# Performance work log

Measured on AMD Instinct MI355X. Metric: run time of the kernel, lower is better.

The kernel has to match this reference:

```python
import jax, jax.numpy as jnp
import numpy as np
import math

B, T, D, S, V = 128, 32, 64, 32, 8192
MAX_REC = 8
PONDER = 0.01
TWO_PI = 2.0 * math.pi


def setup_inputs():
    key = jax.random.key(0)
    ks = jax.random.split(key, 12)
    sd = 1.0 / math.sqrt(D)
    g = lambda k, shape, s: jax.random.normal(k, shape, jnp.float32) * s
    return {
        "x_seq": jax.random.randint(ks[0], (B, T), 0, V),
        "encoder_emb": g(ks[1], (V, 2 * D), 0.02),
        "vq_emb": g(ks[2], (V, 2 * D), sd),
        "norm_rg": jnp.ones((D,), jnp.float32), "norm_rb": jnp.zeros((D,), jnp.float32),
        "norm_ig": jnp.ones((D,), jnp.float32), "norm_ib": jnp.zeros((D,), jnp.float32),
        "qkv_Wr": g(ks[3], (3, D, D), sd), "qkv_br": g(ks[4], (3, D), sd),
        "qkv_Wi": g(ks[5], (3, D, D), sd), "qkv_bi": g(ks[6], (3, D), sd),
        "gate_w": g(ks[7], (2 * D,), sd), "gate_b": jnp.zeros((), jnp.float32),
        "arb_W": g(ks[8], (3, 2 * D), sd), "arb_b": jnp.zeros((3,), jnp.float32),
        "dec_W": g(ks[9], (V, 2 * D), sd), "dec_b": jnp.zeros((V,), jnp.float32),
        "halt_bias": jnp.asarray(3.0, jnp.float32),
        "input_gate": jnp.asarray(0.0, jnp.float32),
    }


def _ln(x, g, b, eps=1e-5):
    mu = x.mean(-1, keepdims=True)
    var = ((x - mu) ** 2).mean(-1, keepdims=True)
    return (x - mu) * jax.lax.rsqrt(var + eps) * g + b


def _forward(x_seq, encoder_emb, vq_emb, norm_rg, norm_rb, norm_ig, norm_ib,
             qkv_Wr, qkv_br, qkv_Wi, qkv_bi, gate_w, gate_b, arb_W, arb_b,
             dec_W, dec_b, halt_bias, input_gate):
    sg = jax.lax.stop_gradient
    e_sq = (vq_emb ** 2).sum(-1)  # [V]
    alpha = jax.nn.sigmoid(input_gate)
    bias = jax.nn.softplus(halt_bias)

    def clin(xr, xi, Wr, br, Wi, bi):
        # torch ComplexLinear: real = fc_r(xr) - fc_i(xi); imag = fc_r(xi) + fc_i(xr)
        return (xr @ Wr.T + br) - (xi @ Wi.T + bi), (xi @ Wr.T + br) + (xr @ Wi.T + bi)

    def mem_write(gr, gi, mr, mi):
        flat = jnp.concatenate([gr, gi], -1)
        wg = jax.nn.sigmoid(flat @ gate_w + gate_b)[:, None, None]  # [B,1,1]
        shr, shi = jnp.roll(mr, 1, axis=1), jnp.roll(mi, 1, axis=1)
        hr = wg * gr[:, None, :] + (1.0 - wg) * shr[:, :1]
        hi = wg * gi[:, None, :] + (1.0 - wg) * shi[:, :1]
        return jnp.concatenate([hr, shr[:, 1:]], 1), jnp.concatenate([hi, shi[:, 1:]], 1)

    def time_step(carry, xt):
        gw_r, gw_i, mem_r, mem_i = carry
        x_r, x_i = xt
        gw_r = alpha * gw_r + (1.0 - alpha) * x_r
        gw_i = alpha * gw_i + (1.0 - alpha) * x_i
        active = jnp.ones((B,), jnp.float32)
        acc_vq = jnp.zeros((B,), jnp.float32)
        acc_ent = jnp.zeros((B,), jnp.float32)
        acc_pond = jnp.zeros((B,), jnp.float32)
        acc_ph = jnp.zeros((B,), jnp.float32)
        fin_idx = jnp.zeros((B,), jnp.int32)
        prev_ang = jnp.arctan2(gw_i, gw_r)
        for _ in range(MAX_REC):
            cr = _ln(gw_r, norm_rg, norm_rb)
            ci = _ln(gw_i, norm_ig, norm_ib)
            z_flat = jnp.concatenate([cr, ci], -1)  # [B,2D]
            # squared-euclidean scores; argmin identical to cdist argmin
            d2 = (z_flat ** 2).sum(-1, keepdims=True) - 2.0 * (z_flat @ vq_emb.T) + e_sq
            idx = jnp.argmin(d2, -1).astype(jnp.int32)
            z_q = vq_emb[idx]
            vq_loss = ((z_q - sg(z_flat)) ** 2).mean(-1) + 0.25 * ((sg(z_q) - z_flat) ** 2).mean(-1)
            z_st = z_flat + sg(z_q - z_flat)  # straight-through
            counts = jnp.zeros((V,), jnp.float32).at[idx].add(1.0) / B
            entropy = -(counts * jnp.log(counts + 1e-10)).sum()
            v_r, v_i = z_st[:, :D], z_st[:, D:]
            # Hermitian gating
            qr, qi = clin(cr, ci, qkv_Wr[0], qkv_br[0], qkv_Wi[0], qkv_bi[0])
            kr, ki = clin(cr, ci, qkv_Wr[1], qkv_br[1], qkv_Wi[1], qkv_bi[1])
            vr2, vi2 = clin(cr, ci, qkv_Wr[2], qkv_br[2], qkv_Wi[2], qkv_bi[2])
            gate = jax.nn.sigmoid((qr * kr + qi * ki).sum(-1, keepdims=True))
            g_r, g_i = vr2 * gate, vi2 * gate
            # memory read (Re<m, q> attention over slots)
            sim = jnp.einsum('bsd,bd->bs', mem_r, cr) + jnp.einsum('bsd,bd->bs', mem_i, ci)
            attn = jax.nn.softmax(sim, -1)
            m_r = jnp.einsum('bs,bsd->bd', attn, mem_r)
            m_i = jnp.einsum('bs,bsd->bd', attn, mem_i)
            gates = jax.nn.softmax(z_flat @ arb_W.T + arb_b, -1)  # [B,3]
            upd_r = gates[:, 0:1] * g_r + gates[:, 1:2] * m_r + gates[:, 2:3] * v_r
            upd_i = gates[:, 0:1] * g_i + gates[:, 1:2] * m_i + gates[:, 2:3] * v_i
            cand_r = 0.6 * cr + 0.4 * upd_r
            cand_i = 0.6 * ci + 0.4 * upd_i
            ang = jnp.arctan2(cand_i, cand_r)
            diff = jnp.abs(ang - prev_ang)
            diff = jnp.minimum(diff, TWO_PI - diff)
            acc_ph = acc_ph + active * diff.mean(-1)
            prev_ang = ang
            halt_prob = jax.nn.sigmoid(bias - vq_loss)
            should_stop = (halt_prob > 0.5).astype(jnp.float32)
            acc_pond = acc_pond + active * PONDER
            mflat = active > 0.5
            acc_vq = jnp.where(mflat, vq_loss, acc_vq)
            acc_ent = jnp.where(mflat, entropy, acc_ent)
            fin_idx = jnp.where(mflat, idx, fin_idx)
            am = mflat[:, None]
            gw_r = jnp.where(am, cand_r, gw_r)
            gw_i = jnp.where(am, cand_i, gw_i)
            active = active * (1.0 - should_stop)
        mem_r, mem_i = mem_write(gw_r, gw_i, mem_r, mem_i)
        stats_t = jnp.stack([acc_vq.mean(), acc_ent.mean(), acc_pond.mean(), acc_ph.mean()])
        return (gw_r, gw_i, mem_r, mem_i), (gw_r, gw_i, fin_idx, stats_t)

    emb = encoder_emb[x_seq]  # [B,T,2D]
    xr = jnp.transpose(emb[..., :D], (1, 0, 2))  # [T,B,D]
    xi = jnp.transpose(emb[..., D:], (1, 0, 2))
    init = (jnp.zeros((B, D), jnp.float32), jnp.zeros((B, D), jnp.float32),
            jnp.zeros((B, S, D), jnp.float32), jnp.zeros((B, S, D), jnp.float32))
    _, (out_r, out_i, idxs, stats) = jax.lax.scan(time_step, init, (xr, xi))
    out = jnp.concatenate([jnp.transpose(out_r, (1, 0, 2)),
                           jnp.transpose(out_i, (1, 0, 2))], -1)  # [B,T,2D]
    logits = out @ dec_W.T + dec_b  # [B,T,V]
    return logits, stats.sum(0) / T, jnp.transpose(idxs)  # [B,T]


def reference(x_seq, encoder_emb, vq_emb, norm_rg, norm_rb, norm_ig, norm_ib, qkv_Wr, qkv_br, qkv_Wi, qkv_bi, gate_w, gate_b, arb_W, arb_b, dec_W, dec_b, halt_bias, input_gate):
    return _forward(x_seq, encoder_emb, vq_emb, norm_rg, norm_rb, norm_ig, norm_ib,
                    qkv_Wr, qkv_br, qkv_Wi, qkv_bi, gate_w, gate_b, arb_W, arb_b,
                    dec_W, dec_b, halt_bias, input_gate)
```

## Files before the change

kernel.cpp:

```cpp
#include <hip/hip_runtime.h>
#include <math.h>

#define TT 32
#define MAXREC 8
#define NBLK 256
#define NTHR 512

#define OFF_ZBUF   0u
#define OFF_ZBUFB  65536u
#define OFF_KEYS   98304u
#define OFF_ZDONE  229376u
#define OFF_ESQ    231424u
#define OFF_RST    264192u
#define OFF_OUTHB  266240u
#define OFF_WB     1314816u

#define SENT 0x7FFFFFFFu
#define IDXM 0x1FFFu
#define LOGN 33554432u
#define TWO_PI_F 6.283185307179586f

typedef float f32x4 __attribute__((ext_vector_type(4)));
typedef short bf16x8 __attribute__((ext_vector_type(8)));
typedef unsigned long long u64;

__device__ __forceinline__ float wredsum(float v) {
#pragma unroll
  for (int m = 32; m > 0; m >>= 1) v += __shfl_xor(v, m);
  return v;
}
__device__ __forceinline__ u64 shflx64(u64 v, int m) {
  int lo = __shfl_xor((int)(unsigned)(v & 0xffffffffull), m);
  int hi = __shfl_xor((int)(unsigned)(v >> 32), m);
  return ((u64)(unsigned)hi << 32) | (unsigned)lo;
}
__device__ __forceinline__ u64 packkey(float d, unsigned c) {
  unsigned u = __float_as_uint(d);
  u = (u & 0x80000000u) ? ~u : (u | 0x80000000u);
  return ((u64)u << 32) | c;
}
__device__ __forceinline__ float unpackd2(u64 key) {
  unsigned hi = (unsigned)(key >> 32);
  unsigned orig = (hi & 0x80000000u) ? (hi & 0x7fffffffu) : ~hi;
  return __uint_as_float(orig);
}
__device__ __forceinline__ unsigned short f2bf(float f) {
  unsigned u = __float_as_uint(f);
  unsigned r = (u >> 16) & 1u;
  u += 0x7fffu + r;
  return (unsigned short)(u >> 16);
}

__device__ __forceinline__ u64 ld_coh64(const u64* p) {
  u64 v;
  asm volatile("global_load_dwordx2 %0, %1, off sc0 sc1\n\ts_waitcnt vmcnt(0)"
               : "=&v"(v) : "v"(p) : "memory");
  return v;
}
__device__ __forceinline__ void st_coh_f32(float* p, float v) {
  asm volatile("global_store_dword %0, %1, off sc0 sc1" :: "v"(p), "v"(v) : "memory");
}
__device__ __forceinline__ void st_coh32(unsigned* p, unsigned v) {
  asm volatile("global_store_dword %0, %1, off sc0 sc1" :: "v"(p), "v"(v) : "memory");
}
__device__ __forceinline__ void st_coh64(u64* p, u64 v) {
  asm volatile("global_store_dwordx2 %0, %1, off sc0 sc1" :: "v"(p), "v"(v) : "memory");
}
__device__ __forceinline__ void drain_vm() {
  asm volatile("s_waitcnt vmcnt(0)" ::: "memory");
}
__device__ __forceinline__ void ld4w(const float* base,
    unsigned o0, unsigned o1, unsigned o2, unsigned o3,
    f32x4& a0, f32x4& a1, f32x4& a2, f32x4& a3) {
  asm volatile(
      "global_load_dwordx4 %0, %4, %8 sc0 sc1\n\t"
      "global_load_dwordx4 %1, %5, %8 sc0 sc1\n\t"
      "global_load_dwordx4 %2, %6, %8 sc0 sc1\n\t"
      "global_load_dwordx4 %3, %7, %8 sc0 sc1\n\t"
      "s_waitcnt vmcnt(0)"
      : "=&v"(a0), "=&v"(a1), "=&v"(a2), "=&v"(a3)
      : "v"(o0), "v"(o1), "v"(o2), "v"(o3), "s"(base)
      : "memory");
}
__device__ __forceinline__ void ld8w(const float* base,
    unsigned o0, unsigned o1, unsigned o2, unsigned o3,
    unsigned o4, unsigned o5, unsigned o6, unsigned o7,
    f32x4& a0, f32x4& a1, f32x4& a2, f32x4& a3,
    f32x4& a4, f32x4& a5, f32x4& a6, f32x4& a7) {
  asm volatile(
      "global_load_dwordx4 %0, %8, %16 sc0 sc1\n\t"
      "global_load_dwordx4 %1, %9, %16 sc0 sc1\n\t"
      "global_load_dwordx4 %2, %10, %16 sc0 sc1\n\t"
      "global_load_dwordx4 %3, %11, %16 sc0 sc1\n\t"
      "global_load_dwordx4 %4, %12, %16 sc0 sc1\n\t"
      "global_load_dwordx4 %5, %13, %16 sc0 sc1\n\t"
      "global_load_dwordx4 %6, %14, %16 sc0 sc1\n\t"
      "global_load_dwordx4 %7, %15, %16 sc0 sc1\n\t"
      "s_waitcnt vmcnt(0)"
      : "=&v"(a0), "=&v"(a1), "=&v"(a2), "=&v"(a3),
        "=&v"(a4), "=&v"(a5), "=&v"(a6), "=&v"(a7)
      : "v"(o0), "v"(o1), "v"(o2), "v"(o3),
        "v"(o4), "v"(o5), "v"(o6), "v"(o7),
        "s"(base)
      : "memory");
}

__global__ __launch_bounds__(512) void sacrsn_init(char* __restrict__ ws) {
  u64* zd = (u64*)(ws + OFF_ZDONE);
  if (threadIdx.x < 256) zd[threadIdx.x] = 0ull;
}

__global__ __launch_bounds__(256) void k_prepv(const float* __restrict__ vqe,
                                               char* __restrict__ ws) {
  unsigned short* vqeB = (unsigned short*)(ws + OFF_WB);
  float* esqG = (float*)(ws + OFF_ESQ);
  const int i = (blockIdx.x * 256 + threadIdx.x) * 4;
  float4 v = *(const float4*)(vqe + i);
  ushort4 o;
  o.x = f2bf(v.x); o.y = f2bf(v.y); o.z = f2bf(v.z); o.w = f2bf(v.w);
  *(ushort4*)(vqeB + i) = o;
  if (blockIdx.x < 32) {
    const int c = blockIdx.x * 256 + threadIdx.x;
    const float4* e = (const float4*)(vqe + ((size_t)c << 7));
    float s = 0.f;
#pragma unroll 8
    for (int k4 = 0; k4 < 32; ++k4) {
      float4 q = e[k4];
      s = fmaf(q.x, q.x, fmaf(q.y, q.y, fmaf(q.z, q.z, fmaf(q.w, q.w, s))));
    }
    esqG[c] = s;
  }
}

__global__ __launch_bounds__(256) void k_prepd(const float* __restrict__ dW,
                                               char* __restrict__ ws) {
  unsigned short* dWb = (unsigned short*)(ws + OFF_WB);
  const int i = (blockIdx.x * 256 + threadIdx.x) * 4;
  float4 v = *(const float4*)(dW + i);
  ushort4 o;
  o.x = f2bf(v.x); o.y = f2bf(v.y); o.z = f2bf(v.z); o.w = f2bf(v.w);
  *(ushort4*)(dWb + i) = o;
}

__global__ __launch_bounds__(NTHR) void sacrsn_main(
    const int* __restrict__ x_seq, const float* __restrict__ enc,
    const float* __restrict__ vqe,
    const float* __restrict__ nrg, const float* __restrict__ nrb,
    const float* __restrict__ nig, const float* __restrict__ nib,
    const float* __restrict__ qWr, const float* __restrict__ qbr,
    const float* __restrict__ qWi, const float* __restrict__ qbi,
    const float* __restrict__ gtw, const float* __restrict__ gtb,
    const float* __restrict__ aW, const float* __restrict__ ab,
    const float* __restrict__ hbp, const float* __restrict__ igp,
    float* __restrict__ dout, char* __restrict__ ws)
{
  float* zbuf = (float*)(ws + OFF_ZBUF);
  unsigned* zbufB32 = (unsigned*)(ws + OFF_ZBUFB);
  u64*   keys = (u64*)(ws + OFF_KEYS);
  u64*   zdone64 = (u64*)(ws + OFF_ZDONE);
  u64*   finalA = (u64*)(ws + OFF_ZDONE + 8u);
  const float* esqG = (const float*)(ws + OFF_ESQ);
  const unsigned short* vqeB = (const unsigned short*)(ws + OFF_WB);
  unsigned short* outhB = (unsigned short*)(ws + OFF_OUTHB);
  float* rst  = (float*)(ws + OFF_RST);

  const int tid = threadIdx.x;
  const int wv = tid >> 6, ln = tid & 63;
  const int blk = blockIdx.x;
  const bool owner = (blk < 128);

  __shared__ float memLr[32 * 65];
  __shared__ float memLi[32 * 65];
  __shared__ float gwrowL[128], pangL[64], zfmL[128], zqL[128];
  __shared__ float qkL[6][64], simL[32], attnL[32], mrL[64], miL[64];
  __shared__ unsigned idxL[128] __attribute__((aligned(16)));
  __shared__ u64 key128L[128], kred[128];
  __shared__ float arbWL[3 * 128];
  __shared__ float scalL[8], entpL[2], vqpL[2], wsumL[2], z2pL[2];
  __shared__ float accL[4], totL[4];
  __shared__ float dmeanS;
  __shared__ u64 actM[2], actN[2];
  __shared__ float z2L[128], sz2L[128];
  __shared__ u64 rowminU[128];
  __shared__ unsigned candL[8192];
  __shared__ unsigned candCount;

  const float alpha = 1.0f / (1.0f + expf(-igp[0]));
  const float onema = 1.0f - alpha;
  const float hbias = log1pf(expf(hbp[0]));
  const float gtb0 = gtb[0];

  if (!owner) {
    const int s = blk - 128;
    const int w = tid >> 6, l = tid & 63;
    const int ar = l & 15, kg = l >> 4;
    const int rowbase = w * 16;
    if (tid < 128) rowminU[tid] = ~0ull;
    if (tid == 0) candCount = 0u;
    __syncthreads();
    unsigned k = 0;
    while (true) {
      u64 tv;
      bool done;
      {
        const u64* tp = &zdone64[(size_t)(rowbase + ar) * 2];
        bool sent;
        while (true) {
          tv = ld_coh64(tp);
          unsigned lo = (unsigned)tv;
          sent = (lo == SENT);
          bool ok = (lo == k + 1u) || sent;
          if (__all(ok)) break;
          __builtin_amdgcn_s_sleep(1);
        }
        done = __any(sent);
      }
      if (done) break;
      {
        float z2 = __uint_as_float((unsigned)(tv >> 32));
        z2L[rowbase + ar] = z2;
        sz2L[rowbase + ar] = sqrtf(z2);
      }
      f32x4 af0, af1, af2, af3;
      {
        const unsigned rb = (unsigned)((rowbase + ar) * 256 + kg * 16);
        ld4w((const float*)(ws + OFF_ZBUFB), rb, rb + 64u, rb + 128u, rb + 192u,
             af0, af1, af2, af3);
      }
      bf16x8 afr[4];
      afr[0] = *(bf16x8*)&af0; afr[1] = *(bf16x8*)&af1;
      afr[2] = *(bf16x8*)&af2; afr[3] = *(bf16x8*)&af3;
      f32x4 dc[4];
#pragma unroll
      for (int nt = 0; nt < 4; ++nt) dc[nt] = (f32x4){0.f, 0.f, 0.f, 0.f};
#pragma unroll
      for (int kc = 0; kc < 4; ++kc) {
#pragma unroll
        for (int nt = 0; nt < 4; ++nt) {
          bf16x8 b = *(const bf16x8*)(vqeB + (((size_t)(s * 64 + nt * 16 + ar)) << 7)
                                      + kc * 32 + kg * 8);
          dc[nt] = __builtin_amdgcn_mfma_f32_16x16x32_bf16(afr[kc], b, dc[nt], 0, 0, 0);
        }
      }
      float aV[4][4], eV[4][4], Lmin[4];
#pragma unroll
      for (int rr = 0; rr < 4; ++rr) Lmin[rr] = 1e30f;
#pragma unroll
      for (int nt = 0; nt < 4; ++nt) {
        const int code = s * 64 + nt * 16 + ar;
        const float es = esqG[code];
        const float se = sqrtf(es);
#pragma unroll
        for (int rr = 0; rr < 4; ++rr) {
          const int row = rowbase + kg * 4 + rr;
          float av = (z2L[row] - 2.0f * dc[nt][rr]) + es;
          float ev = fmaf(0.0082f * sz2L[row], se, 1e-3f);
          aV[nt][rr] = av; eV[nt][rr] = ev;
          float ae = av + ev;
          if (ae < Lmin[rr]) Lmin[rr] = ae;
        }
      }
#pragma unroll
      for (int m2 = 1; m2 < 16; m2 <<= 1)
#pragma unroll
        for (int rr = 0; rr < 4; ++rr) {
          float o = __shfl_xor(Lmin[rr], m2);
          if (o < Lmin[rr]) Lmin[rr] = o;
        }
#pragma unroll
      for (int nt = 0; nt < 4; ++nt)
#pragma unroll
        for (int rr = 0; rr < 4; ++rr)
          if (aV[nt][rr] - eV[nt][rr] <= Lmin[rr]) {
            const unsigned row = (unsigned)(rowbase + kg * 4 + rr);
            const unsigned code = (unsigned)(s * 64 + nt * 16 + ar);
            unsigned pos = atomicAdd(&candCount, 1u);
            candL[pos] = (row << 16) | code;
          }
      __syncthreads();
      const unsigned cnt = candCount;
      for (unsigned base = 0; base < cnt; base += 128u) {
        const unsigned eI = base + (unsigned)(tid >> 2);
        const int sub = tid & 3;
        const bool valid = eI < cnt;
        float dsum = 0.f;
        int row = 0, code = 0;
        if (valid) {
          unsigned en = candL[eI];
          row = (int)(en >> 16); code = (int)(en & 0xFFFFu);
          f32x4 zv0, zv1, zv2, zv3, zv4, zv5, zv6, zv7;
          const unsigned zb = (unsigned)(row * 512 + sub * 128);
          ld8w(zbuf, zb, zb + 16u, zb + 32u, zb + 48u,
               zb + 64u, zb + 80u, zb + 96u, zb + 112u,
               zv0, zv1, zv2, zv3, zv4, zv5, zv6, zv7);
          const float4* ep = (const float4*)(vqe + ((size_t)code << 7) + sub * 32);
          float4 e0 = ep[0], e1 = ep[1], e2 = ep[2], e3 = ep[3];
          float4 e4 = ep[4], e5 = ep[5], e6 = ep[6], e7 = ep[7];
          dsum = fmaf(zv0[0], e0.x, fmaf(zv0[1], e0.y, fmaf(zv0[2], e0.z, fmaf(zv0[3], e0.w, 0.f))));
          dsum = fmaf(zv1[0], e1.x, fmaf(zv1[1], e1.y, fmaf(zv1[2], e1.z, fmaf(zv1[3], e1.w, dsum))));
          dsum = fmaf(zv2[0], e2.x, fmaf(zv2[1], e2.y, fmaf(zv2[2], e2.z, fmaf(zv2[3], e2.w, dsum))));
          dsum = fmaf(zv3[0], e3.x, fmaf(zv3[1], e3.y, fmaf(zv3[2], e3.z, fmaf(zv3[3], e3.w, dsum))));
          dsum = fmaf(zv4[0], e4.x, fmaf(zv4[1], e4.y, fmaf(zv4[2], e4.z, fmaf(zv4[3], e4.w, dsum))));
          dsum = fmaf(zv5[0], e5.x, fmaf(zv5[1], e5.y, fmaf(zv5[2], e5.z, fmaf(zv5[3], e5.w, dsum))));
          dsum = fmaf(zv6[0], e6.x, fmaf(zv6[1], e6.y, fmaf(zv6[2], e6.z, fmaf(zv6[3], e6.w, dsum))));
          dsum = fmaf(zv7[0], e7.x, fmaf(zv7[1], e7.y, fmaf(zv7[2], e7.z, fmaf(zv7[3], e7.w, dsum))));
        }
        dsum += __shfl_xor(dsum, 1);
        dsum += __shfl_xor(dsum, 2);
        if (valid && sub == 0) {
          float d2 = (z2L[row] - 2.0f * dsum) + esqG[code];
          atomicMin(&rowminU[row], packkey(d2, (unsigned)code));
        }
      }
      __syncthreads();
      if (tid < 128) {
        u64 kk = rowminU[tid];
        rowminU[tid] = ~0ull;
        if (tid == 0) candCount = 0u;
        st_coh64(&keys[(size_t)s * 128 + tid], kk | ((u64)(k + 1u) << 13));
      }
      k++;
    }
    return;
  }

  float lnG = 0.0f, lnB = 0.0f, gtwv = 0.0f;
  if (tid < 64) { lnG = nrg[tid]; lnB = nrb[tid]; }
  else if (tid < 128) { lnG = nig[tid - 64]; lnB = nib[tid - 64]; }
  if (tid < 128) gtwv = gtw[tid];
  for (int i = tid; i < 32 * 65; i += NTHR) { memLr[i] = 0.0f; memLi[i] = 0.0f; }
  if (tid < 4) { totL[tid] = 0.0f; accL[tid] = 0.0f; }
  if (tid < 2) actM[tid] = ~0ull;
  for (int i = tid; i < 384; i += NTHR) arbWL[i] = aW[i];
  {
    int tok = x_seq[blk * TT];
    if (tid < 128) gwrowL[tid] = onema * enc[((size_t)tok << 7) + tid];
  }
  __syncthreads();
  if (tid < 64) pangL[tid] = atan2f(gwrowL[64 + tid], gwrowL[tid]);
  if (tid < 128) {
    float val = gwrowL[tid];
    float mu = wredsum(val) * 0.015625f;
    float xc = val - mu;
    float vr = wredsum(xc * xc) * 0.015625f;
    float z = xc * (1.0f / sqrtf(vr + 1e-5f)) * lnG + lnB;
    zfmL[tid] = z;
    st_coh_f32(&zbuf[(blk << 7) + tid], z);
    float zo = __shfl_xor(z, 1);
    if ((tid & 1) == 0) {
      unsigned pk = (unsigned)f2bf(z) | ((unsigned)f2bf(zo) << 16);
      st_coh32(&zbufB32[blk * 64 + (tid >> 1)], pk);
    }
    float s2 = wredsum(z * z);
    if (ln == 0) z2pL[wv] = s2;
  }
  drain_vm();
  __syncthreads();
  if (tid == 0) {
    float z2 = z2pL[0] + z2pL[1];
    st_coh64(&zdone64[blk * 2], (u64)1u | ((u64)__float_as_uint(z2) << 32));
  }

  int t = 0, it = 0;
  unsigned k = 0;
  for (;;) {
    const unsigned tag = k + 1u;
    float encN = 0.0f;
    {
      int tnext = (t + 1 < TT) ? t + 1 : t;
      if (tid < 128) {
        int tk = x_seq[blk * TT + tnext];
        encN = enc[((size_t)tk << 7) + tid];
      }
    }
    if (tid < 192) {
      const int h = tid >> 6, j = tid & 63;
      const float* wr = qWr + h * 4096 + j * 64;
      const float* wi = qWi + h * 4096 + j * 64;
      float da = 0.0f, db_ = 0.0f, dc2 = 0.0f, de = 0.0f;
#pragma unroll 4
      for (int d4 = 0; d4 < 64; d4 += 4) {
        float4 wrv = *(const float4*)&wr[d4];
        float4 wiv = *(const float4*)&wi[d4];
        float4 crv = *(const float4*)&zfmL[d4];
        float4 civ = *(const float4*)&zfmL[64 + d4];
        da = fmaf(crv.x, wrv.x, fmaf(crv.y, wrv.y, fmaf(crv.z, wrv.z, fmaf(crv.w, wrv.w, da))));
        db_ = fmaf(civ.x, wiv.x, fmaf(civ.y, wiv.y, fmaf(civ.z, wiv.z, fmaf(civ.w, wiv.w, db_))));
        dc2 = fmaf(civ.x, wrv.x, fmaf(civ.y, wrv.y, fmaf(civ.z, wrv.z, fmaf(civ.w, wrv.w, dc2))));
        de = fmaf(crv.x, wiv.x, fmaf(crv.y, wiv.y, fmaf(crv.z, wiv.z, fmaf(crv.w, wiv.w, de))));
      }
      float brv = qbr[h * 64 + j], biv = qbi[h * 64 + j];
      qkL[2 * h][j] = da + brv - db_ - biv;
      qkL[2 * h + 1][j] = dc2 + brv + de + biv;
    } else if (tid < 224) {
      const int s2 = tid - 192;
      float a2 = 0.0f;
      for (int d = 0; d < 64; ++d)
        a2 = fmaf(memLr[s2 * 65 + d], zfmL[d], fmaf(memLi[s2 * 65 + d], zfmL[64 + d], a2));
      simL[s2] = a2;
    } else if (tid < 227) {
      const int h = tid - 224;
      float a2 = ab[h];
      for (int k2 = 0; k2 < 128; ++k2) a2 = fmaf(zfmL[k2], arbWL[h * 128 + k2], a2);
      scalL[3 + h] = a2;
    }
    __syncthreads();
    if (tid < 64) {
      float p = fmaf(qkL[0][tid], qkL[2][tid], qkL[1][tid] * qkL[3][tid]);
      p = wredsum(p);
      if (tid == 0) scalL[0] = 1.0f / (1.0f + expf(-p));
    } else if (tid < 96) {
      const int s2 = tid - 64;
      float v = simL[s2];
      float m = v;
#pragma unroll
      for (int msk = 16; msk > 0; msk >>= 1) m = fmaxf(m, __shfl_xor(m, msk));
      float e = expf(v - m);
      float ss = e;
#pragma unroll
      for (int msk = 16; msk > 0; msk >>= 1) ss += __shfl_xor(ss, msk);
      attnL[s2] = e / ss;
    } else if (tid == 96) {
      float a0 = scalL[3], a1 = scalL[4], a2 = scalL[5];
      float m = fmaxf(a0, fmaxf(a1, a2));
      float e0 = expf(a0 - m), e1 = expf(a1 - m), e2 = expf(a2 - m);
      float ssum = e0 + e1 + e2;
      scalL[3] = e0 / ssum; scalL[4] = e1 / ssum; scalL[5] = e2 / ssum;
    }
    __syncthreads();
    if (tid < 128) {
      const int d = ln;
      const float* ml = (wv == 0) ? memLr : memLi;
      float a2 = 0.0f;
#pragma unroll 4
      for (int s2 = 0; s2 < 32; ++s2) a2 = fmaf(attnL[s2], ml[s2 * 65 + d], a2);
      if (wv == 0) mrL[d] = a2; else miL[d] = a2;
    }
    if (tid < 128) {
      const u64* kp = &keys[(size_t)tid * 128 + blk];
      u64 v;
      while (true) {
        v = ld_coh64(kp);
        if (__all(((unsigned)(v >> 13) & 0x7FFFFu) == tag)) break;
        __builtin_amdgcn_s_sleep(1);
      }
      kred[tid] = v;
    }
    __syncthreads();
    if (tid < 64) {
      u64 a = kred[tid], b = kred[tid + 64];
      if (b < a) a = b;
#pragma unroll
      for (int m2 = 32; m2 > 0; m2 >>= 1) { u64 o = shflx64(a, m2); if (o < a) a = o; }
      if (tid == 0) st_coh64(&finalA[blk * 2], a);
    }
    if (tid < 128) {
      const u64* fp = &finalA[(size_t)tid * 2];
      u64 v;
      while (true) {
        v = ld_coh64(fp);
        if (__all(((unsigned)(v >> 13) & 0x7FFFFu) == tag)) break;
        __builtin_amdgcn_s_sleep(1);
      }
      key128L[tid] = v;
    }
    __syncthreads();
    const bool aoldb = ((actM[blk >> 6] >> (blk & 63)) & 1ull) != 0ull;
    if (tid < 128) {
      u64 key = key128L[tid];
      idxL[tid] = (unsigned)key & IDXM;
      float d2 = unpackd2(key);
      bool act_b = ((actM[tid >> 6] >> (tid & 63)) & 1ull) != 0ull;
      bool stop = (1.25f * 0.0078125f * d2) < hbias;
      u64 ball = __ballot(act_b && !stop);
      if (ln == 0) actN[tid >> 6] = ball;
    } else if (tid < 256) {
      const int d = tid - 128;
      unsigned ii2 = (unsigned)key128L[blk] & IDXM;
      float zq = vqe[((size_t)ii2 << 7) + d];
      zqL[d] = zq;
      float df = zq - zfmL[d];
      float sm = wredsum(df * df);
      if (ln == 0) vqpL[wv - 2] = sm;
    }
    __syncthreads();
    const bool anyAct = (actN[0] | actN[1]) != 0ull;
    const bool mf = aoldb;
    if (tid < 2) actM[tid] = actN[tid];
    if (tid < 64) {
      const int d = tid;
      float gate = scalL[0], g0 = scalL[3], g1 = scalL[4], g2 = scalL[5];
      float cr = zfmL[d], ci = zfmL[64 + d];
      float ur = fmaf(g0, qkL[4][d] * gate, fmaf(g1, mrL[d], g2 * zqL[d]));
      float ui = fmaf(g0, qkL[5][d] * gate, fmaf(g1, miL[d], g2 * zqL[64 + d]));
      float cdr = fmaf(0.4f, ur, 0.6f * cr);
      float cdi = fmaf(0.4f, ui, 0.6f * ci);
      mrL[d] = cdr; miL[d] = cdi;
      if (mf) { gwrowL[d] = cdr; gwrowL[64 + d] = cdi; }
    }
    __syncthreads();
    const bool newT = !(anyAct && it < MAXREC - 1);
    const bool finished = newT && (t == TT - 1);
    if (newT && !finished) {
      float pr = 0.0f;
      if (tid < 128) {
        pr = gwrowL[tid];
        outhB[((size_t)blk * TT + t) * 128 + tid] = f2bf(pr);
        float part = wredsum(pr * gtwv);
        if (ln == 0) wsumL[wv] = part;
      }
      __syncthreads();
      if (tid < 128) {
        float wg = 1.0f / (1.0f + expf(-(wsumL[0] + wsumL[1] + gtb0)));
        int slot = 31 - t;
        float* m = (tid < 64) ? &memLr[slot * 65 + tid] : &memLi[slot * 65 + (tid - 64)];
        *m = fmaf(wg, pr, (1.0f - wg) * (*m));
        gwrowL[tid] = fmaf(alpha, pr, onema * encN);
      }
      __syncthreads();
    }
    if (!finished) {
      if (tid < 128) {
        float val = gwrowL[tid];
        float mu = wredsum(val) * 0.015625f;
        float xc = val - mu;
        float vr = wredsum(xc * xc) * 0.015625f;
        float z = xc * (1.0f / sqrtf(vr + 1e-5f)) * lnG + lnB;
        zfmL[tid] = z;
        st_coh_f32(&zbuf[(blk << 7) + tid], z);
        float zo = __shfl_xor(z, 1);
        if ((tid & 1) == 0) {
          unsigned pk = (unsigned)f2bf(z) | ((unsigned)f2bf(zo) << 16);
          st_coh32(&zbufB32[blk * 64 + (tid >> 1)], pk);
        }
        float s2 = wredsum(z * z);
        if (ln == 0) z2pL[wv] = s2;
      }
      drain_vm();
      __syncthreads();
      if (tid == 0) {
        float z2 = z2pL[0] + z2pL[1];
        st_coh64(&zdone64[blk * 2], (u64)(k + 2u) | ((u64)__float_as_uint(z2) << 32));
      }
    } else {
      __syncthreads();
    }
    if (tid < 64) {
      const int d = tid;
      float cdr = mrL[d], cdi = miL[d];
      float ang = atan2f(cdi, cdr);
      float df = fabsf(ang - pangL[d]);
      df = fminf(df, TWO_PI_F - df);
      pangL[d] = ang;
      float dm = wredsum(df) * 0.015625f;
      if (d == 0) dmeanS = dm;
    } else if (tid >= 128 && tid < 256) {
      const int r = tid - 128;
      unsigned my = idxL[r];
      int c = 0;
#pragma unroll
      for (int j4 = 0; j4 < 32; ++j4) {
        uint4 q = *(const uint4*)&idxL[j4 * 4];
        c += (q.x == my) + (q.y == my) + (q.z == my) + (q.w == my);
      }
      float term = -0.0078125f * logf((float)c * 0.0078125f + 1e-10f);
      term = wredsum(term);
      if (ln == 0) entpL[wv - 2] = term;
    }
    __syncthreads();
    if (tid == 0) {
      float aold = mf ? 1.0f : 0.0f;
      float vql = 1.25f * (vqpL[0] + vqpL[1]) * 0.0078125f;
      accL[3] += aold * dmeanS;
      accL[2] += aold * 0.01f;
      if (mf) {
        accL[0] = vql;
        accL[1] = entpL[0] + entpL[1];
        dout[(size_t)LOGN + 4 + (size_t)blk * TT + t] = (float)idxL[blk];
      }
    }
    if (newT && !finished) {
      if (tid < 64) pangL[tid] = atan2f(gwrowL[64 + tid], gwrowL[tid]);
      if (tid < 4) { totL[tid] += accL[tid]; accL[tid] = 0.0f; }
      if (tid < 2) actM[tid] = ~0ull;
    }
    __syncthreads();
    if (finished) break;
    if (newT) { t++; it = 0; } else { it++; }
    k++;
  }

  if (tid < 128) outhB[((size_t)blk * TT + (TT - 1)) * 128 + tid] = f2bf(gwrowL[tid]);
  if (tid < 4) rst[blk * 4 + tid] = totL[tid] + accL[tid];
  __syncthreads();
  if (tid == 0) st_coh64(&zdone64[blk * 2], (u64)SENT);
}

__global__ __launch_bounds__(256) void k_dec(
    const float* __restrict__ dbv, float* __restrict__ dout,
    const char* __restrict__ ws)
{
  const unsigned short* outhB = (const unsigned short*)(ws + OFF_OUTHB);
  const unsigned short* dWb = (const unsigned short*)(ws + OFF_WB);
  const float* rst = (const float*)(ws + OFF_RST);
  const int tid = threadIdx.x;
  if (blockIdx.x == 0 && tid < 4) {
    float s = 0.0f;
    for (int r = 0; r < 128; ++r) s += rst[r * 4 + tid];
    dout[(size_t)LOGN + tid] = s * (1.0f / 4096.0f);
  }
  const int w = tid >> 6, l = tid & 63;
  const int bm = blockIdx.x & 63;
  const int bn = blockIdx.x >> 6;
  const int ar = l & 15, kg = l >> 4;
  const int m_base = bm * 64;
  const int n_base = bn * 256 + w * 64;
  f32x4 acc[4][4];
#pragma unroll
  for (int mt = 0; mt < 4; ++mt)
#pragma unroll
    for (int nt = 0; nt < 4; ++nt) acc[mt][nt] = (f32x4){0.f, 0.f, 0.f, 0.f};
#pragma unroll
  for (int kc = 0; kc < 4; ++kc) {
    const int ko = kc * 32 + kg * 8;
    bf16x8 a[4], b[4];
#pragma unroll
    for (int mt = 0; mt < 4; ++mt)
      a[mt] = *(const bf16x8*)(outhB + (size_t)(m_base + mt * 16 + ar) * 128 + ko);
#pragma unroll
    for (int nt = 0; nt < 4; ++nt)
      b[nt] = *(const bf16x8*)(dWb + (size_t)(n_base + nt * 16 + ar) * 128 + ko);
#pragma unroll
    for (int mt = 0; mt < 4; ++mt)
#pragma unroll
      for (int nt = 0; nt < 4; ++nt)
        acc[mt][nt] = __builtin_amdgcn_mfma_f32_16x16x32_bf16(a[mt], b[nt], acc[mt][nt], 0, 0, 0);
  }
#pragma unroll
  for (int nt = 0; nt < 4; ++nt) {
    const int n = n_base + nt * 16 + ar;
    const float bv = dbv[n];
#pragma unroll
    for (int mt = 0; mt < 4; ++mt) {
#pragma unroll
      for (int rr = 0; rr < 4; ++rr) {
        const int m = m_base + mt * 16 + kg * 4 + rr;
        dout[(size_t)m * 8192 + n] = acc[mt][nt][rr] + bv;
      }
    }
  }
}

extern "C" void kernel_launch(void* const* d_in, const int* in_sizes, int n_in,
                              void* d_out, int out_size, void* d_ws, size_t ws_size,
                              hipStream_t stream) {
  (void)in_sizes; (void)n_in; (void)out_size; (void)ws_size;
  const int*   x_seq = (const int*)d_in[0];
  const float* enc = (const float*)d_in[1];
  const float* vq  = (const float*)d_in[2];
  const float* nrg = (const float*)d_in[3];
  const float* nrb = (const float*)d_in[4];
  const float* nig = (const float*)d_in[5];
  const float* nib = (const float*)d_in[6];
  const float* qWr = (const float*)d_in[7];
  const float* qbr = (const float*)d_in[8];
  const float* qWi = (const float*)d_in[9];
  const float* qbi = (const float*)d_in[10];
  const float* gtw = (const float*)d_in[11];
  const float* gtb = (const float*)d_in[12];
  const float* aW  = (const float*)d_in[13];
  const float* ab  = (const float*)d_in[14];
  const float* dW  = (const float*)d_in[15];
  const float* db  = (const float*)d_in[16];
  const float* hb  = (const float*)d_in[17];
  const float* ig  = (const float*)d_in[18];
  char* ws = (char*)d_ws;
  float* out = (float*)d_out;
  hipLaunchKernelGGL(sacrsn_init, dim3(1), dim3(512), 0, stream, ws);
  hipLaunchKernelGGL(k_prepv, dim3(1024), dim3(256), 0, stream, vq, ws);
  hipLaunchKernelGGL(sacrsn_main, dim3(NBLK), dim3(NTHR), 0, stream,
                     x_seq, enc, vq, nrg, nrb, nig, nib, qWr, qbr, qWi, qbi,
                     gtw, gtb, aW, ab, hb, ig, out, ws);
  hipLaunchKernelGGL(k_prepd, dim3(1024), dim3(256), 0, stream, dW, ws);
  hipLaunchKernelGGL(k_dec, dim3(2048), dim3(256), 0, stream, db, out, ws);
}
```

Measured before the change: 721.4 us.

## Speculatively start next timestep before global halt decision resolves

Owner blocks now predict that the halting loop ends each step and build and publish the next timestep's normalized state before waiting on the all-block halting consensus. This takes one cross-block barrier round trip off the critical path of the common case. On a misprediction the block rebuilds the recurrence state and republishes it under a skipped tag. The init kernel also clears the keys buffer, and the searcher blocks accept tags at or beyond the expected one. Mispredictions add extra work and tag bookkeeping, and the protocol is fragile.

```diff
diff --git a/kernel.cpp b/kernel.cpp
--- a/kernel.cpp
+++ b/kernel.cpp
@@ -107,7 +107,14 @@
 
 __global__ __launch_bounds__(512) void sacrsn_init(char* __restrict__ ws) {
   u64* zd = (u64*)(ws + OFF_ZDONE);
-  if (threadIdx.x < 256) zd[threadIdx.x] = 0ull;
+  u64* keys = (u64*)(ws + OFF_KEYS);
+  const int g = blockIdx.x * 512 + threadIdx.x;
+  if (blockIdx.x == 0 && threadIdx.x < 256) zd[threadIdx.x] = 0ull;
+#pragma unroll
+  for (int j = 0; j < 1; ++j) {
+    int i = g;
+    if (i < 16384) keys[i] = 0ull;
+  }
 }
 
 __global__ __launch_bounds__(256) void k_prepv(const float* __restrict__ vqe,
@@ -179,6 +186,7 @@
   __shared__ float scalL[8], entpL[2], vqpL[2], wsumL[2], z2pL[2];
   __shared__ float accL[4], totL[4];
   __shared__ float dmeanS;
+  __shared__ unsigned iiS;
   __shared__ u64 actM[2], actN[2];
   __shared__ float z2L[128], sz2L[128];
   __shared__ u64 rowminU[128];
@@ -209,7 +217,7 @@
           tv = ld_coh64(tp);
           unsigned lo = (unsigned)tv;
           sent = (lo == SENT);
-          bool ok = (lo == k + 1u) || sent;
+          bool ok = sent || ((int)(lo - (k + 1u)) >= 0);
           if (__all(ok)) break;
           __builtin_amdgcn_s_sleep(1);
         }
@@ -362,9 +370,8 @@
   }
 
   int t = 0, it = 0;
-  unsigned k = 0;
+  unsigned k = 1;
   for (;;) {
-    const unsigned tag = k + 1u;
     float encN = 0.0f;
     {
       int tnext = (t + 1 < TT) ? t + 1 : t;
@@ -441,7 +448,7 @@
       u64 v;
       while (true) {
         v = ld_coh64(kp);
-        if (__all(((unsigned)(v >> 13) & 0x7FFFFu) == tag)) break;
+        if (__all(((unsigned)(v >> 13) & 0x7FFFFu) == k)) break;
         __builtin_amdgcn_s_sleep(1);
       }
       kred[tid] = v;
@@ -452,41 +459,19 @@
       if (b < a) a = b;
 #pragma unroll
       for (int m2 = 32; m2 > 0; m2 >>= 1) { u64 o = shflx64(a, m2); if (o < a) a = o; }
-      if (tid == 0) st_coh64(&finalA[blk * 2], a);
-    }
+      if (tid == 0) { st_coh64(&finalA[blk * 2], a); iiS = (unsigned)a & IDXM; }
+    }
+    __syncthreads();
+    const unsigned ii = iiS;
+    const bool mf = ((actM[blk >> 6] >> (blk & 63)) & 1ull) != 0ull;
     if (tid < 128) {
-      const u64* fp = &finalA[(size_t)tid * 2];
-      u64 v;
-      while (true) {
-        v = ld_coh64(fp);
-        if (__all(((unsigned)(v >> 13) & 0x7FFFFu) == tag)) break;
-        __builtin_amdgcn_s_sleep(1);
-      }
-      key128L[tid] = v;
-    }
-    __syncthreads();
-    const bool aoldb = ((actM[blk >> 6] >> (blk & 63)) & 1ull) != 0ull;
-    if (tid < 128) {
-      u64 key = key128L[tid];
-      idxL[tid] = (unsigned)key & IDXM;
-      float d2 = unpackd2(key);
-      bool act_b = ((actM[tid >> 6] >> (tid & 63)) & 1ull) != 0ull;
-      bool stop = (1.25f * 0.0078125f * d2) < hbias;
-      u64 ball = __ballot(act_b && !stop);
-      if (ln == 0) actN[tid >> 6] = ball;
-    } else if (tid < 256) {
-      const int d = tid - 128;
-      unsigned ii2 = (unsigned)key128L[blk] & IDXM;
-      float zq = vqe[((size_t)ii2 << 7) + d];
-      zqL[d] = zq;
-      float df = zq - zfmL[d];
+      float zq = vqe[((size_t)ii << 7) + tid];
+      float df = zq - zfmL[tid];
       float sm = wredsum(df * df);
-      if (ln == 0) vqpL[wv - 2] = sm;
-    }
-    __syncthreads();
-    const bool anyAct = (actN[0] | actN[1]) != 0ull;
-    const bool mf = aoldb;
-    if (tid < 2) actM[tid] = actN[tid];
+      if (ln == 0) vqpL[wv] = sm;
+      zqL[tid] = zq;
+    }
+    __syncthreads();
     if (tid < 64) {
       const int d = tid;
       float gate = scalL[0], g0 = scalL[3], g1 = scalL[4], g2 = scalL[5];
@@ -496,34 +481,99 @@
       float cdr = fmaf(0.4f, ur, 0.6f * cr);
       float cdi = fmaf(0.4f, ui, 0.6f * ci);
       mrL[d] = cdr; miL[d] = cdi;
-      if (mf) { gwrowL[d] = cdr; gwrowL[64 + d] = cdi; }
-    }
-    __syncthreads();
-    const bool newT = !(anyAct && it < MAXREC - 1);
-    const bool finished = newT && (t == TT - 1);
-    if (newT && !finished) {
-      float pr = 0.0f;
-      if (tid < 128) {
-        pr = gwrowL[tid];
-        outhB[((size_t)blk * TT + t) * 128 + tid] = f2bf(pr);
-        float part = wredsum(pr * gtwv);
-        if (ln == 0) wsumL[wv] = part;
-      }
+      zqL[d]      = mf ? cdr : gwrowL[d];
+      zqL[64 + d] = mf ? cdi : gwrowL[64 + d];
+    }
+    __syncthreads();
+    const bool specMerge = (t < TT - 1);
+    if (tid < 128) {
+      float g = specMerge ? fmaf(alpha, zqL[tid], onema * encN) : zqL[tid];
+      float mu = wredsum(g) * 0.015625f;
+      float xc = g - mu;
+      float vr = wredsum(xc * xc) * 0.015625f;
+      float z = xc * (1.0f / sqrtf(vr + 1e-5f)) * lnG + lnB;
+      zfmL[tid] = z;
+      st_coh_f32(&zbuf[(blk << 7) + tid], z);
+      float zo = __shfl_xor(z, 1);
+      if ((tid & 1) == 0) {
+        unsigned pk = (unsigned)f2bf(z) | ((unsigned)f2bf(zo) << 16);
+        st_coh32(&zbufB32[blk * 64 + (tid >> 1)], pk);
+      }
+      float s2 = wredsum(z * z);
+      if (ln == 0) z2pL[wv] = s2;
+    }
+    drain_vm();
+    __syncthreads();
+    if (tid == 0) {
+      float z2 = z2pL[0] + z2pL[1];
+      st_coh64(&zdone64[blk * 2], (u64)(k + 1u) | ((u64)__float_as_uint(z2) << 32));
+    }
+    if (tid < 128) {
+      const u64* fp = &finalA[(size_t)tid * 2];
+      u64 v;
+      while (true) {
+        v = ld_coh64(fp);
+        if (__all(((unsigned)(v >> 13) & 0x7FFFFu) == k)) break;
+        __builtin_amdgcn_s_sleep(1);
+      }
+      key128L[tid] = v;
+    }
+    __syncthreads();
+    if (tid < 128) {
+      u64 key = key128L[tid];
+      idxL[tid] = (unsigned)key & IDXM;
+      float d2 = unpackd2(key);
+      bool act_b = ((actM[tid >> 6] >> (tid & 63)) & 1ull) != 0ull;
+      bool stop = (1.25f * 0.0078125f * d2) < hbias;
+      u64 ball = __ballot(act_b && !stop);
+      if (ln == 0) actN[tid >> 6] = ball;
+    }
+    __syncthreads();
+    const bool anyAct = (actN[0] | actN[1]) != 0ull;
+    const bool actualNewT = (!anyAct) || (it == MAXREC - 1);
+    const bool mispredict = !actualNewT;
+    const bool finished = actualNewT && (t == TT - 1);
+    if (tid < 64) {
+      const int d = tid;
+      float ang = atan2f(miL[d], mrL[d]);
+      float df = fabsf(ang - pangL[d]);
+      df = fminf(df, TWO_PI_F - df);
+      pangL[d] = ang;
+      float dm = wredsum(df) * 0.015625f;
+      if (d == 0) dmeanS = dm;
+    } else if (tid >= 128 && tid < 256) {
+      const int r = tid - 128;
+      unsigned my = idxL[r];
+      int c = 0;
+#pragma unroll
+      for (int j4 = 0; j4 < 32; ++j4) {
+        uint4 q = *(const uint4*)&idxL[j4 * 4];
+        c += (q.x == my) + (q.y == my) + (q.z == my) + (q.w == my);
+      }
+      float term = -0.0078125f * logf((float)c * 0.0078125f + 1e-10f);
+      term = wredsum(term);
+      if (ln == 0) entpL[wv - 2] = term;
+    }
+    __syncthreads();
+    if (tid == 0) {
+      float aold = mf ? 1.0f : 0.0f;
+      accL[3] += aold * dmeanS;
+      accL[2] += aold * 0.01f;
+      if (mf) {
+        accL[0] = 1.25f * (vqpL[0] + vqpL[1]) * 0.0078125f;
+        accL[1] = entpL[0] + entpL[1];
+        dout[(size_t)LOGN + 4 + (size_t)blk * TT + t] = (float)ii;
+      }
+    }
+    if (tid < 2) actM[tid] = actN[tid];
+    __syncthreads();
+    if (mispredict) {
+      if (tid < 128) gwrowL[tid] = zqL[tid];
       __syncthreads();
       if (tid < 128) {
-        float wg = 1.0f / (1.0f + expf(-(wsumL[0] + wsumL[1] + gtb0)));
-        int slot = 31 - t;
-        float* m = (tid < 64) ? &memLr[slot * 65 + tid] : &memLi[slot * 65 + (tid - 64)];
-        *m = fmaf(wg, pr, (1.0f - wg) * (*m));
-        gwrowL[tid] = fmaf(alpha, pr, onema * encN);
-      }
-      __syncthreads();
-    }
-    if (!finished) {
-      if (tid < 128) {
-        float val = gwrowL[tid];
-        float mu = wredsum(val) * 0.015625f;
-        float xc = val - mu;
+        float g = gwrowL[tid];
+        float mu = wredsum(g) * 0.015625f;
+        float xc = g - mu;
         float vr = wredsum(xc * xc) * 0.015625f;
         float z = xc * (1.0f / sqrtf(vr + 1e-5f)) * lnG + lnB;
         zfmL[tid] = z;
@@ -542,55 +592,37 @@
         float z2 = z2pL[0] + z2pL[1];
         st_coh64(&zdone64[blk * 2], (u64)(k + 2u) | ((u64)__float_as_uint(z2) << 32));
       }
-    } else {
       __syncthreads();
-    }
-    if (tid < 64) {
-      const int d = tid;
-      float cdr = mrL[d], cdi = miL[d];
-      float ang = atan2f(cdi, cdr);
-      float df = fabsf(ang - pangL[d]);
-      df = fminf(df, TWO_PI_F - df);
-      pangL[d] = ang;
-      float dm = wredsum(df) * 0.015625f;
-      if (d == 0) dmeanS = dm;
-    } else if (tid >= 128 && tid < 256) {
-      const int r = tid - 128;
-      unsigned my = idxL[r];
-      int c = 0;
-#pragma unroll
-      for (int j4 = 0; j4 < 32; ++j4) {
-        uint4 q = *(const uint4*)&idxL[j4 * 4];
-        c += (q.x == my) + (q.y == my) + (q.z == my) + (q.w == my);
-      }
-      float term = -0.0078125f * logf((float)c * 0.0078125f + 1e-10f);
-      term = wredsum(term);
-      if (ln == 0) entpL[wv - 2] = term;
-    }
-    __syncthreads();
-    if (tid == 0) {
-      float aold = mf ? 1.0f : 0.0f;
-      float vql = 1.25f * (vqpL[0] + vqpL[1]) * 0.0078125f;
-      accL[3] += aold * dmeanS;
-      accL[2] += aold * 0.01f;
-      if (mf) {
-        accL[0] = vql;
-        accL[1] = entpL[0] + entpL[1];
-        dout[(size_t)LOGN + 4 + (size_t)blk * TT + t] = (float)idxL[blk];
-      }
-    }
-    if (newT && !finished) {
+      k += 2; it += 1;
+      continue;
+    }
+    if (finished) break;
+    {
+      float pr = 0.0f;
+      if (tid < 128) {
+        pr = zqL[tid];
+        outhB[((size_t)blk * TT + t) * 128 + tid] = f2bf(pr);
+        float part = wredsum(pr * gtwv);
+        if (ln == 0) wsumL[wv] = part;
+      }
+      __syncthreads();
+      if (tid < 128) {
+        float wg = 1.0f / (1.0f + expf(-(wsumL[0] + wsumL[1] + gtb0)));
+        int slot = 31 - t;
+        float* m = (tid < 64) ? &memLr[slot * 65 + tid] : &memLi[slot * 65 + (tid - 64)];
+        *m = fmaf(wg, pr, (1.0f - wg) * (*m));
+        gwrowL[tid] = fmaf(alpha, pr, onema * encN);
+      }
+      __syncthreads();
       if (tid < 64) pangL[tid] = atan2f(gwrowL[64 + tid], gwrowL[tid]);
       if (tid < 4) { totL[tid] += accL[tid]; accL[tid] = 0.0f; }
       if (tid < 2) actM[tid] = ~0ull;
-    }
-    __syncthreads();
-    if (finished) break;
-    if (newT) { t++; it = 0; } else { it++; }
-    k++;
-  }
-
-  if (tid < 128) outhB[((size_t)blk * TT + (TT - 1)) * 128 + tid] = f2bf(gwrowL[tid]);
+      __syncthreads();
+    }
+    t++; it = 0; k += 1;
+  }
+
+  if (tid < 128) outhB[((size_t)blk * TT + (TT - 1)) * 128 + tid] = f2bf(zqL[tid]);
   if (tid < 4) rst[blk * 4 + tid] = totL[tid] + accL[tid];
   __syncthreads();
   if (tid == 0) st_coh64(&zdone64[blk * 2], (u64)SENT);
@@ -676,7 +708,7 @@
   const float* ig  = (const float*)d_in[18];
   char* ws = (char*)d_ws;
   float* out = (float*)d_out;
-  hipLaunchKernelGGL(sacrsn_init, dim3(1), dim3(512), 0, stream, ws);
+  hipLaunchKernelGGL(sacrsn_init, dim3(32), dim3(512), 0, stream, ws);
   hipLaunchKernelGGL(k_prepv, dim3(1024), dim3(256), 0, stream, vq, ws);
   hipLaunchKernelGGL(sacrsn_main, dim3(NBLK), dim3(NTHR), 0, stream,
                      x_seq, enc, vq, nrg, nrb, nig, nib, qWr, qbr, qWi, qbi,
```

After: 678.1 us. 6.0% less time.
